# Kernel tuning notes

Measured on AMD Instinct MI355X. Metric: run time of the kernel, lower is better.

Reference implementation:

```python
import jax, jax.numpy as jnp
import numpy as np

TEMPERATURE = 0.07
MARGIN = 0.2
SHUF_ID_OFFSET = 100000


def _normalize(x):
    # matches F.normalize(x + 1e-8, dim=-1) with default eps=1e-12
    v = x + 1e-8
    n = jnp.linalg.norm(v, axis=-1, keepdims=True)
    return v / jnp.maximum(n, 1e-12)


def setup_inputs() -> dict:
    key = jax.random.key(0)
    k1, k2, k3, k4 = jax.random.split(key, 4)
    M, C, D = 1024, 3, 512
    return {
        "motion_embs": jax.random.normal(k1, (M, D), dtype=jnp.float32),
        "text_embs": jax.random.normal(k2, (M, C, D), dtype=jnp.float32),
        "shuffled_text_embs": jax.random.normal(k3, (M, C, D), dtype=jnp.float32),
        "motion_ids": jax.random.randint(k4, (M,), 0, 256, dtype=jnp.int64 if jax.config.jax_enable_x64 else jnp.int32),
    }


def reference(motion_embs, text_embs, shuffled_text_embs, motion_ids):
    M, C, D = text_embs.shape
    m = _normalize(motion_embs)                       # [M, D]
    t = _normalize(text_embs).reshape(M * C, D)       # [M*C, D]
    s = _normalize(shuffled_text_embs).reshape(M * C, D)

    emb = jnp.concatenate([m, t, s], axis=0)          # [N, D], N = M + 2*M*C
    ids = jnp.concatenate([
        motion_ids,
        jnp.repeat(motion_ids, C),
        jnp.repeat(motion_ids + SHUF_ID_OFFSET, C),
    ])

    sim = (emb @ emb.T) / TEMPERATURE                 # [N, N]
    N = emb.shape[0]
    same = ids[None, :] == ids[:, None]
    eye = jnp.eye(N, dtype=bool)
    pos_mask = same & ~eye
    neg_mask = (~same) & ~eye

    exp_sim = jnp.exp(sim)
    # denominator over positives + negatives (all off-diagonal), as in the original
    denom = jnp.sum(jnp.where(pos_mask | neg_mask, exp_sim, 0.0), axis=1)   # [N]
    n_pos = jnp.sum(pos_mask, axis=1)
    n_neg = jnp.sum(neg_mask, axis=1)

    pos_sum = jnp.sum(jnp.where(pos_mask, sim, 0.0), axis=1)
    infonce = jnp.log(denom) - pos_sum / jnp.maximum(n_pos, 1)               # [N]

    margin = jnp.sum(jnp.where(neg_mask, jnp.maximum(sim + MARGIN, 0.0), 0.0), axis=1) / jnp.maximum(n_neg, 1)

    valid = (n_pos > 0) & (n_neg > 0)
    count = jnp.sum(valid)
    total = jnp.sum(jnp.where(valid, infonce + margin, 0.0))
    loss = jnp.where(count > 0, total / jnp.maximum(count, 1), 0.0)
    return loss
```

## Files before the change

kernel.cpp:

```cpp
#include <hip/hip_runtime.h>

#define M_ROWS 1024
#define DIM 512
#define NB 1024
#define N_TOT 7168
#define TEXT_OFF 1024
#define SHUF_OFF 4096
#define INV_T (1.0f/0.07f)
#define MARGIN_V 0.2f
#define TILES2 28
#define NBLK2 406
#define SLOT 1536

typedef __attribute__((ext_vector_type(8))) short bf16x8;
typedef __attribute__((ext_vector_type(4))) float f32x4;

typedef const __attribute__((address_space(1))) unsigned int gas_uint;
typedef __attribute__((address_space(3))) unsigned int las_uint;

__device__ __forceinline__ void gload16(const void* g, void* l) {
  __builtin_amdgcn_global_load_lds((gas_uint*)g, (las_uint*)l, 16, 0, 0);
}

__device__ __forceinline__ ushort f2bf(float f) {
  unsigned u = __float_as_uint(f);
  u += 0x7fffu + ((u >> 16) & 1u);
  return (ushort)(u >> 16);
}

__device__ __forceinline__ float dpp_sum16(float x) {
  float s = x;
  s += __int_as_float(__builtin_amdgcn_update_dpp(0, __float_as_int(s), 0x111, 0xF, 0xF, true));
  s += __int_as_float(__builtin_amdgcn_update_dpp(0, __float_as_int(s), 0x112, 0xF, 0xF, true));
  s += __int_as_float(__builtin_amdgcn_update_dpp(0, __float_as_int(s), 0x114, 0xF, 0xF, true));
  s += __int_as_float(__builtin_amdgcn_update_dpp(0, __float_as_int(s), 0x118, 0xF, 0xF, true));
  return s;
}

__global__ __launch_bounds__(256) void k_normalize(
    const float* __restrict__ motion, const float* __restrict__ text,
    const float* __restrict__ shuf, const int* __restrict__ mids,
    ushort* __restrict__ emb, int* __restrict__ ids) {
  int wave = threadIdx.x >> 6;
  int lane = threadIdx.x & 63;
  int row = blockIdx.x * 4 + wave;
  if (row >= N_TOT) return;
  const float* src;
  int id;
  if (row < TEXT_OFF) { src = motion + (size_t)row * DIM; id = mids[row]; }
  else if (row < SHUF_OFF) { int r = row - TEXT_OFF; src = text + (size_t)r * DIM; id = mids[r / 3]; }
  else { int r = row - SHUF_OFF; src = shuf + (size_t)r * DIM; id = mids[r / 3] + 100000; }

  float4 a = ((const float4*)src)[lane * 2];
  float4 b = ((const float4*)src)[lane * 2 + 1];
  float v0 = a.x + 1e-8f, v1 = a.y + 1e-8f, v2 = a.z + 1e-8f, v3 = a.w + 1e-8f;
  float v4 = b.x + 1e-8f, v5 = b.y + 1e-8f, v6 = b.z + 1e-8f, v7 = b.w + 1e-8f;
  float ss = v0*v0 + v1*v1 + v2*v2 + v3*v3 + v4*v4 + v5*v5 + v6*v6 + v7*v7;
  #pragma unroll
  for (int m = 1; m < 64; m <<= 1) ss += __shfl_xor(ss, m);
  float inv = 1.0f / fmaxf(sqrtf(ss), 1e-12f);

  uint w0 = (uint)f2bf(v0 * inv) | ((uint)f2bf(v1 * inv) << 16);
  uint w1 = (uint)f2bf(v2 * inv) | ((uint)f2bf(v3 * inv) << 16);
  uint w2 = (uint)f2bf(v4 * inv) | ((uint)f2bf(v5 * inv) << 16);
  uint w3 = (uint)f2bf(v6 * inv) | ((uint)f2bf(v7 * inv) << 16);
  uint4 pk; pk.x = w0; pk.y = w1; pk.z = w2; pk.w = w3;
  *((uint4*)(emb + (size_t)row * DIM + lane * 8)) = pk;
  if (lane == 0) ids[row] = id;
}

__global__ __launch_bounds__(512, 2) void k_gemm_loss(
    const ushort* __restrict__ emb, const int* __restrict__ ids,
    float* __restrict__ part) {
  __shared__ ushort Asm[3][8192];
  __shared__ ushort Bsm[3][8192];

  int orig = blockIdx.x;
  int xcd = orig & 7;
  int idx = orig >> 3;
  int bid = (xcd < 6 ? xcd * 51 : 306 + (xcd - 6) * 50) + idx;

  int x = 0;
  while (bid >= TILES2 - x) { bid -= TILES2 - x; x++; }
  int y = x + bid;
  bool diag = (x == y);
  int brow = x * 256, bcol = y * 256;
  int tbid = x * TILES2 - x * (x - 1) / 2 + (y - x);

  int t = threadIdx.x;
  int l = t & 63;
  int w = t >> 6;
  int wr = w >> 2;
  int wc = w & 3;
  int fr = l & 15;
  int fg = l >> 4;

  int srow = w * 16 + (l >> 2);
  int scol = ((l & 3) ^ ((l >> 3) & 3)) * 16;
  const char* gA = (const char*)emb + (size_t)(brow + srow) * NB + scol;
  const char* gB = (const char*)emb + (size_t)(bcol + srow) * NB + scol;
  int ldso = w * 512;

  f32x4 acc[8][4];
  #pragma unroll
  for (int m = 0; m < 8; m++)
    #pragma unroll
    for (int n = 0; n < 4; n++)
      acc[m][n] = (f32x4){0.f, 0.f, 0.f, 0.f};

  int swz = (fg ^ ((fr >> 1) & 3)) * 8;

#define STAGE(T) do { \
    const int _b = (T) % 3; const int _kb = (T) * 64; \
    gload16(gA + _kb,          &Asm[_b][ldso]); \
    gload16(gA + 131072 + _kb, &Asm[_b][4096 + ldso]); \
    gload16(gB + _kb,          &Bsm[_b][ldso]); \
    gload16(gB + 131072 + _kb, &Bsm[_b][4096 + ldso]); \
  } while (0)

  STAGE(0);
  STAGE(1);
  asm volatile("s_waitcnt vmcnt(4)" ::: "memory");
  __builtin_amdgcn_s_barrier();

  #pragma unroll
  for (int tt = 0; tt < 16; tt++) {
    if (tt + 2 < 16) STAGE(tt + 2);
    const int _b = tt % 3;
    const ushort* Ab = &Asm[_b][(wr * 128 + fr) * 32 + swz];
    const ushort* Bb = &Bsm[_b][(wc * 64 + fr) * 32 + swz];
    bf16x8 aF[8], bF[4];
    #pragma unroll
    for (int m = 0; m < 8; m++) aF[m] = *(const bf16x8*)(Ab + m * 512);
    #pragma unroll
    for (int n = 0; n < 4; n++) bF[n] = *(const bf16x8*)(Bb + n * 512);
    __builtin_amdgcn_s_setprio(1);
    #pragma unroll
    for (int m = 0; m < 8; m++)
      #pragma unroll
      for (int n = 0; n < 4; n++)
        acc[m][n] = __builtin_amdgcn_mfma_f32_16x16x32_bf16(aF[m], bF[n], acc[m][n], 0, 0, 0);
    __builtin_amdgcn_s_setprio(0);
    if (tt < 14) {
      asm volatile("s_waitcnt vmcnt(4)" ::: "memory");
      __builtin_amdgcn_s_barrier();
    } else if (tt == 14) {
      asm volatile("s_waitcnt vmcnt(0)" ::: "memory");
      __builtin_amdgcn_s_barrier();
    }
  }
#undef STAGE

  float* rpd = (float*)&Asm[0][0];
  float* rpp = rpd + 1024;
  float* rpm = rpp + 1024;
  float* cps = (float*)&Bsm[0][0];
  int* ridL = (int*)&Bsm[1][0];
  int* cidL = ridL + 256;
  if (t < 256) ridL[t] = ids[brow + t];
  else cidL[t - 256] = ids[bcol + (t - 256)];
  __syncthreads();

  float* ps = part + (size_t)tbid * SLOT;

  int cl = fr;
  int cgrp = fg;
  int cidv[4];
  #pragma unroll
  for (int n = 0; n < 4; n++) cidv[n] = cidL[wc * 64 + n * 16 + cl];
  float cd[4], cp[4], cm[4];
  #pragma unroll
  for (int n = 0; n < 4; n++) { cd[n] = 0.f; cp[n] = 0.f; cm[n] = 0.f; }

  #pragma unroll
  for (int m = 0; m < 8; m++) {
    #pragma unroll
    for (int r = 0; r < 4; r++) {
      int row_l = wr * 128 + m * 16 + cgrp * 4 + r;
      int i = brow + row_l;
      int idi = ridL[row_l];
      float dsum = 0.f, psum = 0.f, msum = 0.f;
      #pragma unroll
      for (int n = 0; n < 4; n++) {
        int col_l = wc * 64 + n * 16 + cl;
        int j = bcol + col_l;
        float sim = acc[m][n][r] * INV_T;
        bool live = (!diag) || (i != j);
        if (live) {
          float e = __expf(sim);
          float hinge = fmaxf(sim + MARGIN_V, 0.f);
          bool same = (idi == cidv[n]);
          float psv = same ? sim : 0.f;
          float msv = same ? 0.f : hinge;
          dsum += e; psum += psv; msum += msv;
          if (!diag) { cd[n] += e; cp[n] += psv; cm[n] += msv; }
        }
      }
      dsum = dpp_sum16(dsum);
      psum = dpp_sum16(psum);
      msum = dpp_sum16(msum);
      if (cl == 15) {
        int o = w * 128 + (row_l & 127);
        rpd[o] = dsum; rpp[o] = psum; rpm[o] = msum;
      }
    }
  }

  if (!diag) {
    #pragma unroll
    for (int n = 0; n < 4; n++) {
      float d = cd[n], p = cp[n], mm = cm[n];
      d += __shfl_xor(d, 16); d += __shfl_xor(d, 32);
      p += __shfl_xor(p, 16); p += __shfl_xor(p, 32);
      mm += __shfl_xor(mm, 16); mm += __shfl_xor(mm, 32);
      if (l < 16) {
        int o = ((w * 4 + n) * 16 + cl) * 3;
        cps[o] = d; cps[o + 1] = p; cps[o + 2] = mm;
      }
    }
  }
  __syncthreads();

  if (t < 256) {
    int b0 = (t >> 7) * 512 + (t & 127);
    float d = rpd[b0] + rpd[b0 + 128] + rpd[b0 + 256] + rpd[b0 + 384];
    float p = rpp[b0] + rpp[b0 + 128] + rpp[b0 + 256] + rpp[b0 + 384];
    float mm = rpm[b0] + rpm[b0 + 128] + rpm[b0 + 256] + rpm[b0 + 384];
    ps[t] = d; ps[256 + t] = p; ps[512 + t] = mm;
  }
  if (!diag && wr == 0 && l < 16) {
    #pragma unroll
    for (int n = 0; n < 4; n++) {
      int o0 = ((w * 4 + n) * 16 + cl) * 3;
      int o1 = (((w + 4) * 4 + n) * 16 + cl) * 3;
      int col_l = wc * 64 + n * 16 + cl;
      ps[768 + col_l] = cps[o0] + cps[o1];
      ps[768 + 256 + col_l] = cps[o0 + 1] + cps[o1 + 1];
      ps[768 + 512 + col_l] = cps[o0 + 2] + cps[o1 + 2];
    }
  }
}

__global__ __launch_bounds__(256) void k_reduce(
    const float* __restrict__ part, const int* __restrict__ mids,
    float* __restrict__ blockout) {
  __shared__ int hist[256];
  __shared__ float reds[256];
  __shared__ int redc[256];
  int t = threadIdx.x;
  hist[t] = 0;
  __syncthreads();
  for (int i = t; i < M_ROWS; i += 256) atomicAdd(&hist[mids[i]], 1);
  __syncthreads();

  int p = blockIdx.x;
  int i = p * 256 + t;
  float d = 0.f, pp = 0.f, mm = 0.f;
  int base = p * TILES2 - p * (p - 1) / 2;
  for (int yy = p; yy < TILES2; yy++) {
    const float* s = part + (size_t)(base + yy - p) * SLOT;
    d += s[t]; pp += s[256 + t]; mm += s[512 + t];
  }
  for (int xx = 0; xx < p; xx++) {
    int b = xx * TILES2 - xx * (xx - 1) / 2 + (p - xx);
    const float* s = part + (size_t)b * SLOT + 768;
    d += s[t]; pp += s[256 + t]; mm += s[512 + t];
  }

  int vmid; bool sh = false;
  if (i < TEXT_OFF) vmid = mids[i];
  else if (i < SHUF_OFF) vmid = mids[(i - TEXT_OFF) / 3];
  else { vmid = mids[(i - SHUF_OFF) / 3]; sh = true; }
  int c = hist[vmid];
  int npos = sh ? (3 * c - 1) : (4 * c - 1);
  int nneg = N_TOT - 1 - npos;
  float val = 0.f; int cnt = 0;
  if (npos > 0 && nneg > 0) {
    val = logf(d) - pp / (float)(npos > 1 ? npos : 1) + mm / (float)(nneg > 1 ? nneg : 1);
    cnt = 1;
  }
  reds[t] = val; redc[t] = cnt;
  __syncthreads();
  for (int s2 = 128; s2 > 0; s2 >>= 1) {
    if (t < s2) { reds[t] += reds[t + s2]; redc[t] += redc[t + s2]; }
    __syncthreads();
  }
  if (t == 0) { blockout[p * 2] = reds[0]; blockout[p * 2 + 1] = (float)redc[0]; }
}

__global__ __launch_bounds__(64) void k_final(
    const float* __restrict__ blockout, float* __restrict__ out) {
  int t = threadIdx.x;
  float s = 0.f, c = 0.f;
  if (t < TILES2) { s = blockout[t * 2]; c = blockout[t * 2 + 1]; }
  #pragma unroll
  for (int m = 32; m > 0; m >>= 1) { s += __shfl_down(s, m); c += __shfl_down(c, m); }
  if (t == 0) out[0] = (c > 0.f) ? s / c : 0.f;
}

extern "C" void kernel_launch(void* const* d_in, const int* in_sizes, int n_in,
                              void* d_out, int out_size, void* d_ws, size_t ws_size,
                              hipStream_t stream) {
  const float* motion = (const float*)d_in[0];
  const float* text   = (const float*)d_in[1];
  const float* shuf   = (const float*)d_in[2];
  const int*   mids   = (const int*)d_in[3];

  char* ws = (char*)d_ws;
  ushort* emb = (ushort*)ws;
  int* ids    = (int*)(ws + (size_t)N_TOT * DIM * 2);
  float* blockout = (float*)(ws + 7368704);
  float* part = (float*)(ws + 7454720);

  k_normalize<<<N_TOT / 4, 256, 0, stream>>>(motion, text, shuf, mids, emb, ids);
  k_gemm_loss<<<NBLK2, 512, 0, stream>>>(emb, ids, part);
  k_reduce<<<TILES2, 256, 0, stream>>>(part, mids, blockout);
  k_final<<<1, 64, 0, stream>>>(blockout, (float*)d_out);
}
```

Before: 74.42 us.

## Shrink GEMM tiles to 128x128 and fuse final reduction via ticket

Halves the symmetric-GEMM tile from 256x256 to 128x128, giving 1596 upper-triangle blocks of 256 threads instead of 406 blocks of 512. This improves load balance and wave coverage across CUs at the cost of less operand reuse per block and more partial-sum traffic. It also folds the final scalar reduction into k_reduce using an atomic ticket, which is reset in k_normalize, so one kernel launch is removed.

```diff
diff --git a/kernel.cpp b/kernel.cpp
--- a/kernel.cpp
+++ b/kernel.cpp
@@ -8,9 +8,9 @@
 #define SHUF_OFF 4096
 #define INV_T (1.0f/0.07f)
 #define MARGIN_V 0.2f
-#define TILES2 28
-#define NBLK2 406
-#define SLOT 1536
+#define TILES 56
+#define NBLK 1596
+#define SLOT 768
 
 typedef __attribute__((ext_vector_type(8))) short bf16x8;
 typedef __attribute__((ext_vector_type(4))) float f32x4;
@@ -40,7 +40,8 @@
 __global__ __launch_bounds__(256) void k_normalize(
     const float* __restrict__ motion, const float* __restrict__ text,
     const float* __restrict__ shuf, const int* __restrict__ mids,
-    ushort* __restrict__ emb, int* __restrict__ ids) {
+    ushort* __restrict__ emb, int* __restrict__ ids, int* __restrict__ ticket) {
+  if (blockIdx.x == 0 && threadIdx.x == 0) *ticket = 0;
   int wave = threadIdx.x >> 6;
   int lane = threadIdx.x & 63;
   int row = blockIdx.x * 4 + wave;
@@ -69,29 +70,29 @@
   if (lane == 0) ids[row] = id;
 }
 
-__global__ __launch_bounds__(512, 2) void k_gemm_loss(
+__global__ __launch_bounds__(256, 3) void k_gemm_loss(
     const ushort* __restrict__ emb, const int* __restrict__ ids,
     float* __restrict__ part) {
-  __shared__ ushort Asm[3][8192];
-  __shared__ ushort Bsm[3][8192];
+  __shared__ ushort Asm[3][4096];
+  __shared__ ushort Bsm[3][4096];
 
   int orig = blockIdx.x;
   int xcd = orig & 7;
   int idx = orig >> 3;
-  int bid = (xcd < 6 ? xcd * 51 : 306 + (xcd - 6) * 50) + idx;
+  int bid = (xcd < 4 ? xcd * 200 : 800 + (xcd - 4) * 199) + idx;
 
   int x = 0;
-  while (bid >= TILES2 - x) { bid -= TILES2 - x; x++; }
+  while (bid >= TILES - x) { bid -= TILES - x; x++; }
   int y = x + bid;
   bool diag = (x == y);
-  int brow = x * 256, bcol = y * 256;
-  int tbid = x * TILES2 - x * (x - 1) / 2 + (y - x);
+  int brow = x * 128, bcol = y * 128;
+  int tbid = x * TILES - x * (x - 1) / 2 + (y - x);
 
   int t = threadIdx.x;
   int l = t & 63;
   int w = t >> 6;
-  int wr = w >> 2;
-  int wc = w & 3;
+  int wr = w >> 1;
+  int wc = w & 1;
   int fr = l & 15;
   int fg = l >> 4;
 
@@ -101,9 +102,9 @@
   const char* gB = (const char*)emb + (size_t)(bcol + srow) * NB + scol;
   int ldso = w * 512;
 
-  f32x4 acc[8][4];
-  #pragma unroll
-  for (int m = 0; m < 8; m++)
+  f32x4 acc[4][4];
+  #pragma unroll
+  for (int m = 0; m < 4; m++)
     #pragma unroll
     for (int n = 0; n < 4; n++)
       acc[m][n] = (f32x4){0.f, 0.f, 0.f, 0.f};
@@ -112,10 +113,10 @@
 
 #define STAGE(T) do { \
     const int _b = (T) % 3; const int _kb = (T) * 64; \
-    gload16(gA + _kb,          &Asm[_b][ldso]); \
-    gload16(gA + 131072 + _kb, &Asm[_b][4096 + ldso]); \
-    gload16(gB + _kb,          &Bsm[_b][ldso]); \
-    gload16(gB + 131072 + _kb, &Bsm[_b][4096 + ldso]); \
+    gload16(gA + _kb,         &Asm[_b][ldso]); \
+    gload16(gA + 65536 + _kb, &Asm[_b][2048 + ldso]); \
+    gload16(gB + _kb,         &Bsm[_b][ldso]); \
+    gload16(gB + 65536 + _kb, &Bsm[_b][2048 + ldso]); \
   } while (0)
 
   STAGE(0);
@@ -127,16 +128,16 @@
   for (int tt = 0; tt < 16; tt++) {
     if (tt + 2 < 16) STAGE(tt + 2);
     const int _b = tt % 3;
-    const ushort* Ab = &Asm[_b][(wr * 128 + fr) * 32 + swz];
+    const ushort* Ab = &Asm[_b][(wr * 64 + fr) * 32 + swz];
     const ushort* Bb = &Bsm[_b][(wc * 64 + fr) * 32 + swz];
-    bf16x8 aF[8], bF[4];
-    #pragma unroll
-    for (int m = 0; m < 8; m++) aF[m] = *(const bf16x8*)(Ab + m * 512);
+    bf16x8 aF[4], bF[4];
+    #pragma unroll
+    for (int m = 0; m < 4; m++) aF[m] = *(const bf16x8*)(Ab + m * 512);
     #pragma unroll
     for (int n = 0; n < 4; n++) bF[n] = *(const bf16x8*)(Bb + n * 512);
     __builtin_amdgcn_s_setprio(1);
     #pragma unroll
-    for (int m = 0; m < 8; m++)
+    for (int m = 0; m < 4; m++)
       #pragma unroll
       for (int n = 0; n < 4; n++)
         acc[m][n] = __builtin_amdgcn_mfma_f32_16x16x32_bf16(aF[m], bF[n], acc[m][n], 0, 0, 0);
@@ -151,14 +152,15 @@
   }
 #undef STAGE
 
-  float* rpd = (float*)&Asm[0][0];
-  float* rpp = rpd + 1024;
-  float* rpm = rpp + 1024;
-  float* cps = (float*)&Bsm[0][0];
-  int* ridL = (int*)&Bsm[1][0];
-  int* cidL = ridL + 256;
-  if (t < 256) ridL[t] = ids[brow + t];
-  else cidL[t - 256] = ids[bcol + (t - 256)];
+  __syncthreads();
+  float* rpd = (float*)&Asm[1][0];
+  float* rpp = rpd + 256;
+  float* rpm = rpp + 256;
+  float* cps = (float*)&Bsm[1][0];
+  int* ridL = (int*)&Asm[2][0];
+  int* cidL = ridL + 128;
+  if (t < 128) ridL[t] = ids[brow + t];
+  else cidL[t - 128] = ids[bcol + (t - 128)];
   __syncthreads();
 
   float* ps = part + (size_t)tbid * SLOT;
@@ -173,10 +175,10 @@
   for (int n = 0; n < 4; n++) { cd[n] = 0.f; cp[n] = 0.f; cm[n] = 0.f; }
 
   #pragma unroll
-  for (int m = 0; m < 8; m++) {
+  for (int m = 0; m < 4; m++) {
     #pragma unroll
     for (int r = 0; r < 4; r++) {
-      int row_l = wr * 128 + m * 16 + cgrp * 4 + r;
+      int row_l = wr * 64 + m * 16 + cgrp * 4 + r;
       int i = brow + row_l;
       int idi = ridL[row_l];
       float dsum = 0.f, psum = 0.f, msum = 0.f;
@@ -200,7 +202,7 @@
       psum = dpp_sum16(psum);
       msum = dpp_sum16(msum);
       if (cl == 15) {
-        int o = w * 128 + (row_l & 127);
+        int o = w * 64 + (row_l & 63);
         rpd[o] = dsum; rpp[o] = psum; rpm[o] = msum;
       }
     }
@@ -221,50 +223,52 @@
   }
   __syncthreads();
 
-  if (t < 256) {
-    int b0 = (t >> 7) * 512 + (t & 127);
-    float d = rpd[b0] + rpd[b0 + 128] + rpd[b0 + 256] + rpd[b0 + 384];
-    float p = rpp[b0] + rpp[b0 + 128] + rpp[b0 + 256] + rpp[b0 + 384];
-    float mm = rpm[b0] + rpm[b0 + 128] + rpm[b0 + 256] + rpm[b0 + 384];
-    ps[t] = d; ps[256 + t] = p; ps[512 + t] = mm;
+  if (t < 128) {
+    int b0 = (t >> 6) * 128 + (t & 63);
+    float d = rpd[b0] + rpd[b0 + 64];
+    float p = rpp[b0] + rpp[b0 + 64];
+    float mm = rpm[b0] + rpm[b0 + 64];
+    ps[t] = d; ps[128 + t] = p; ps[256 + t] = mm;
   }
   if (!diag && wr == 0 && l < 16) {
     #pragma unroll
     for (int n = 0; n < 4; n++) {
       int o0 = ((w * 4 + n) * 16 + cl) * 3;
-      int o1 = (((w + 4) * 4 + n) * 16 + cl) * 3;
-      int col_l = wc * 64 + n * 16 + cl;
-      ps[768 + col_l] = cps[o0] + cps[o1];
-      ps[768 + 256 + col_l] = cps[o0 + 1] + cps[o1 + 1];
-      ps[768 + 512 + col_l] = cps[o0 + 2] + cps[o1 + 2];
-    }
-  }
-}
-
-__global__ __launch_bounds__(256) void k_reduce(
+      int o1 = (((w + 2) * 4 + n) * 16 + cl) * 3;
+      int col_l = w * 64 + n * 16 + cl;
+      ps[384 + col_l] = cps[o0] + cps[o1];
+      ps[384 + 128 + col_l] = cps[o0 + 1] + cps[o1 + 1];
+      ps[384 + 256 + col_l] = cps[o0 + 2] + cps[o1 + 2];
+    }
+  }
+}
+
+__global__ __launch_bounds__(128) void k_reduce(
     const float* __restrict__ part, const int* __restrict__ mids,
-    float* __restrict__ blockout) {
+    float* __restrict__ blockout, int* __restrict__ ticket,
+    float* __restrict__ out) {
   __shared__ int hist[256];
-  __shared__ float reds[256];
-  __shared__ int redc[256];
+  __shared__ float reds[128];
+  __shared__ int redc[128];
+  __shared__ int lastf;
   int t = threadIdx.x;
-  hist[t] = 0;
-  __syncthreads();
-  for (int i = t; i < M_ROWS; i += 256) atomicAdd(&hist[mids[i]], 1);
+  hist[t] = 0; hist[t + 128] = 0;
+  __syncthreads();
+  for (int i = t; i < M_ROWS; i += 128) atomicAdd(&hist[mids[i]], 1);
   __syncthreads();
 
   int p = blockIdx.x;
-  int i = p * 256 + t;
+  int i = p * 128 + t;
   float d = 0.f, pp = 0.f, mm = 0.f;
-  int base = p * TILES2 - p * (p - 1) / 2;
-  for (int yy = p; yy < TILES2; yy++) {
+  int base = p * TILES - p * (p - 1) / 2;
+  for (int yy = p; yy < TILES; yy++) {
     const float* s = part + (size_t)(base + yy - p) * SLOT;
-    d += s[t]; pp += s[256 + t]; mm += s[512 + t];
+    d += s[t]; pp += s[128 + t]; mm += s[256 + t];
   }
   for (int xx = 0; xx < p; xx++) {
-    int b = xx * TILES2 - xx * (xx - 1) / 2 + (p - xx);
-    const float* s = part + (size_t)b * SLOT + 768;
-    d += s[t]; pp += s[256 + t]; mm += s[512 + t];
+    int b = xx * TILES - xx * (xx - 1) / 2 + (p - xx);
+    const float* s = part + (size_t)b * SLOT + 384;
+    d += s[t]; pp += s[128 + t]; mm += s[256 + t];
   }
 
   int vmid; bool sh = false;
@@ -281,21 +285,30 @@
   }
   reds[t] = val; redc[t] = cnt;
   __syncthreads();
-  for (int s2 = 128; s2 > 0; s2 >>= 1) {
+  for (int s2 = 64; s2 > 0; s2 >>= 1) {
     if (t < s2) { reds[t] += reds[t + s2]; redc[t] += redc[t + s2]; }
     __syncthreads();
   }
-  if (t == 0) { blockout[p * 2] = reds[0]; blockout[p * 2 + 1] = (float)redc[0]; }
-}
-
-__global__ __launch_bounds__(64) void k_final(
-    const float* __restrict__ blockout, float* __restrict__ out) {
-  int t = threadIdx.x;
-  float s = 0.f, c = 0.f;
-  if (t < TILES2) { s = blockout[t * 2]; c = blockout[t * 2 + 1]; }
-  #pragma unroll
-  for (int m = 32; m > 0; m >>= 1) { s += __shfl_down(s, m); c += __shfl_down(c, m); }
-  if (t == 0) out[0] = (c > 0.f) ? s / c : 0.f;
+  if (t == 0) {
+    blockout[p * 2] = reds[0];
+    blockout[p * 2 + 1] = (float)redc[0];
+    __threadfence();
+    int old = atomicAdd(ticket, 1);
+    lastf = (old == TILES - 1);
+  }
+  __syncthreads();
+  if (lastf) {
+    __threadfence();
+    float s = (t < TILES) ? blockout[t * 2] : 0.f;
+    float cc = (t < TILES) ? blockout[t * 2 + 1] : 0.f;
+    reds[t] = s; redc[t] = (int)cc;
+    __syncthreads();
+    for (int s2 = 64; s2 > 0; s2 >>= 1) {
+      if (t < s2) { reds[t] += reds[t + s2]; redc[t] += redc[t + s2]; }
+      __syncthreads();
+    }
+    if (t == 0) out[0] = (redc[0] > 0) ? reds[0] / (float)redc[0] : 0.f;
+  }
 }
 
 extern "C" void kernel_launch(void* const* d_in, const int* in_sizes, int n_in,
@@ -308,12 +321,12 @@
 
   char* ws = (char*)d_ws;
   ushort* emb = (ushort*)ws;
-  int* ids    = (int*)(ws + (size_t)N_TOT * DIM * 2);
+  int* ids    = (int*)(ws + 7340032);
   float* blockout = (float*)(ws + 7368704);
-  float* part = (float*)(ws + 7454720);
-
-  k_normalize<<<N_TOT / 4, 256, 0, stream>>>(motion, text, shuf, mids, emb, ids);
-  k_gemm_loss<<<NBLK2, 512, 0, stream>>>(emb, ids, part);
-  k_reduce<<<TILES2, 256, 0, stream>>>(part, mids, blockout);
-  k_final<<<1, 64, 0, stream>>>(blockout, (float*)d_out);
-}
+  int* ticket = (int*)(ws + 7369216);
+  float* part = (float*)(ws + 7372800);
+
+  k_normalize<<<N_TOT / 4, 256, 0, stream>>>(motion, text, shuf, mids, emb, ids, ticket);
+  k_gemm_loss<<<NBLK, 256, 0, stream>>>(emb, ids, part);
+  k_reduce<<<TILES, 128, 0, stream>>>(part, mids, blockout, ticket, (float*)d_out);
+}
```

Result: slower. 81.14 us (+9.0%).

## Restructure GEMM mainloop into K=128 double-buffered stages with interleaved quarter-MFMA schedule

Applied to the files above, without the earlier changes.

Replaces the 3-stage K=64 LDS ring with a 2-stage double buffer of K=128 tiles, split into halves, and issues global-to-LDS loads for the next tile between quarter-sized MFMA groups separated by barriers. The aim is finer interleaving of memory loads with matrix work and fewer barrier/waitcnt rounds per K step. LDS use rises to 128KB, so launch bounds drop to one block per CU, trading occupancy for deeper in-block pipelining. The swizzle is widened to 8 chunks to match the new 128-element row layout.

```diff
diff --git a/kernel.cpp b/kernel.cpp
--- a/kernel.cpp
+++ b/kernel.cpp
@@ -69,11 +69,11 @@
   if (lane == 0) ids[row] = id;
 }
 
-__global__ __launch_bounds__(512, 2) void k_gemm_loss(
+__global__ __launch_bounds__(512, 1) void k_gemm_loss(
     const ushort* __restrict__ emb, const int* __restrict__ ids,
     float* __restrict__ part) {
-  __shared__ ushort Asm[3][8192];
-  __shared__ ushort Bsm[3][8192];
+  __shared__ ushort Asm[2][2][8192];
+  __shared__ ushort Bsm[2][2][8192];
 
   int orig = blockIdx.x;
   int xcd = orig & 7;
@@ -95,11 +95,10 @@
   int fr = l & 15;
   int fg = l >> 4;
 
-  int srow = w * 16 + (l >> 2);
-  int scol = ((l & 3) ^ ((l >> 3) & 3)) * 16;
-  const char* gA = (const char*)emb + (size_t)(brow + srow) * NB + scol;
-  const char* gB = (const char*)emb + (size_t)(bcol + srow) * NB + scol;
-  int ldso = w * 512;
+  int srow = w * 8 + (l >> 3);
+  int sgb = ((l & 7) ^ ((l >> 3) & 7)) * 16;
+  const char* gAr = (const char*)emb + (size_t)(brow + srow) * NB + sgb;
+  const char* gBr = (const char*)emb + (size_t)(bcol + srow) * NB + sgb;
 
   f32x4 acc[8][4];
   #pragma unroll
@@ -108,54 +107,96 @@
     for (int n = 0; n < 4; n++)
       acc[m][n] = (f32x4){0.f, 0.f, 0.f, 0.f};
 
-  int swz = (fg ^ ((fr >> 1) & 3)) * 8;
-
-#define STAGE(T) do { \
-    const int _b = (T) % 3; const int _kb = (T) * 64; \
-    gload16(gA + _kb,          &Asm[_b][ldso]); \
-    gload16(gA + 131072 + _kb, &Asm[_b][4096 + ldso]); \
-    gload16(gB + _kb,          &Bsm[_b][ldso]); \
-    gload16(gB + 131072 + _kb, &Bsm[_b][4096 + ldso]); \
+  int sw0 = ((fg) ^ (fr & 7)) * 8;
+  int sw1 = ((4 + fg) ^ (fr & 7)) * 8;
+
+#define STAGE_A(H, KT) do { \
+    gload16(gAr + (size_t)(H) * 131072 + (KT) * 128,         &Asm[(KT) & 1][H][w * 512]); \
+    gload16(gAr + (size_t)(H) * 131072 + 65536 + (KT) * 128, &Asm[(KT) & 1][H][4096 + w * 512]); \
   } while (0)
-
-  STAGE(0);
-  STAGE(1);
-  asm volatile("s_waitcnt vmcnt(4)" ::: "memory");
-  __builtin_amdgcn_s_barrier();
-
-  #pragma unroll
-  for (int tt = 0; tt < 16; tt++) {
-    if (tt + 2 < 16) STAGE(tt + 2);
-    const int _b = tt % 3;
-    const ushort* Ab = &Asm[_b][(wr * 128 + fr) * 32 + swz];
-    const ushort* Bb = &Bsm[_b][(wc * 64 + fr) * 32 + swz];
-    bf16x8 aF[8], bF[4];
-    #pragma unroll
-    for (int m = 0; m < 8; m++) aF[m] = *(const bf16x8*)(Ab + m * 512);
-    #pragma unroll
-    for (int n = 0; n < 4; n++) bF[n] = *(const bf16x8*)(Bb + n * 512);
-    __builtin_amdgcn_s_setprio(1);
-    #pragma unroll
-    for (int m = 0; m < 8; m++)
-      #pragma unroll
-      for (int n = 0; n < 4; n++)
-        acc[m][n] = __builtin_amdgcn_mfma_f32_16x16x32_bf16(aF[m], bF[n], acc[m][n], 0, 0, 0);
-    __builtin_amdgcn_s_setprio(0);
-    if (tt < 14) {
-      asm volatile("s_waitcnt vmcnt(4)" ::: "memory");
-      __builtin_amdgcn_s_barrier();
-    } else if (tt == 14) {
-      asm volatile("s_waitcnt vmcnt(0)" ::: "memory");
-      __builtin_amdgcn_s_barrier();
-    }
-  }
-#undef STAGE
-
-  float* rpd = (float*)&Asm[0][0];
+#define STAGE_B(H, KT) do { \
+    gload16(gBr + (size_t)(H) * 131072 + (KT) * 128,         &Bsm[(KT) & 1][H][w * 512]); \
+    gload16(gBr + (size_t)(H) * 131072 + 65536 + (KT) * 128, &Bsm[(KT) & 1][H][4096 + w * 512]); \
+  } while (0)
+
+  bf16x8 aF[4][2], bF0[2][2], bF1[2][2];
+
+#define LOAD_A(KT, MH) do { \
+    const ushort* AH = &Asm[(KT) & 1][wr][0]; \
+    _Pragma("unroll") \
+    for (int mi = 0; mi < 4; mi++) { \
+      int ro = (((MH) * 4 + mi) * 16 + fr) * 64; \
+      aF[mi][0] = *(const bf16x8*)(AH + ro + sw0); \
+      aF[mi][1] = *(const bf16x8*)(AH + ro + sw1); \
+    } } while (0)
+#define LOAD_B(KT, NH, DST) do { \
+    const ushort* BH = &Bsm[(KT) & 1][wc >> 1][0]; \
+    _Pragma("unroll") \
+    for (int ni = 0; ni < 2; ni++) { \
+      int ro = ((wc & 1) * 64 + ((NH) * 2 + ni) * 16 + fr) * 64; \
+      DST[ni][0] = *(const bf16x8*)(BH + ro + sw0); \
+      DST[ni][1] = *(const bf16x8*)(BH + ro + sw1); \
+    } } while (0)
+#define MFMA_Q(MH, NH, BSRC) do { \
+    __builtin_amdgcn_s_setprio(1); \
+    _Pragma("unroll") \
+    for (int ks = 0; ks < 2; ks++) \
+      _Pragma("unroll") \
+      for (int mi = 0; mi < 4; mi++) \
+        _Pragma("unroll") \
+        for (int ni = 0; ni < 2; ni++) \
+          acc[(MH) * 4 + mi][(NH) * 2 + ni] = __builtin_amdgcn_mfma_f32_16x16x32_bf16( \
+              aF[mi][ks], BSRC[ni][ks], acc[(MH) * 4 + mi][(NH) * 2 + ni], 0, 0, 0); \
+    __builtin_amdgcn_s_setprio(0); \
+  } while (0)
+#define BAR() __builtin_amdgcn_s_barrier()
+#define DRAIN() do { asm volatile("s_waitcnt vmcnt(0)" ::: "memory"); __builtin_amdgcn_s_barrier(); } while (0)
+
+  STAGE_A(0, 0); STAGE_A(1, 0); STAGE_B(0, 0); STAGE_B(1, 0);
+  DRAIN();
+
+  #pragma unroll
+  for (int it = 0; it < 4; it++) {
+    const int ka = 2 * it, kb = 2 * it + 1;
+    LOAD_A(ka, 0); LOAD_B(ka, 0, bF0);
+    STAGE_A(0, kb);
+    BAR(); MFMA_Q(0, 0, bF0); BAR();
+    LOAD_B(ka, 1, bF1);
+    STAGE_A(1, kb);
+    BAR(); MFMA_Q(0, 1, bF1); BAR();
+    LOAD_A(ka, 1);
+    STAGE_B(0, kb);
+    BAR(); MFMA_Q(1, 0, bF0); BAR();
+    STAGE_B(1, kb);
+    BAR(); MFMA_Q(1, 1, bF1);
+    DRAIN();
+    LOAD_A(kb, 0); LOAD_B(kb, 0, bF0);
+    if (it < 3) STAGE_A(0, ka + 2);
+    BAR(); MFMA_Q(0, 0, bF0); BAR();
+    LOAD_B(kb, 1, bF1);
+    if (it < 3) STAGE_A(1, ka + 2);
+    BAR(); MFMA_Q(0, 1, bF1); BAR();
+    LOAD_A(kb, 1);
+    if (it < 3) STAGE_B(0, ka + 2);
+    BAR(); MFMA_Q(1, 0, bF0); BAR();
+    if (it < 3) STAGE_B(1, ka + 2);
+    BAR(); MFMA_Q(1, 1, bF1);
+    DRAIN();
+  }
+#undef STAGE_A
+#undef STAGE_B
+#undef LOAD_A
+#undef LOAD_B
+#undef MFMA_Q
+#undef BAR
+#undef DRAIN
+
+  __syncthreads();
+  float* rpd = (float*)&Asm[0][0][0];
   float* rpp = rpd + 1024;
   float* rpm = rpp + 1024;
-  float* cps = (float*)&Bsm[0][0];
-  int* ridL = (int*)&Bsm[1][0];
+  float* cps = (float*)&Bsm[0][0][0];
+  int* ridL = (int*)&Bsm[1][0][0];
   int* cidL = ridL + 256;
   if (t < 256) ridL[t] = ids[brow + t];
   else cidL[t - 256] = ids[bcol + (t - 256)];
@@ -308,7 +349,7 @@
 
   char* ws = (char*)d_ws;
   ushort* emb = (ushort*)ws;
-  int* ids    = (int*)(ws + (size_t)N_TOT * DIM * 2);
+  int* ids    = (int*)(ws + 7340032);
   float* blockout = (float*)(ws + 7368704);
   float* part = (float*)(ws + 7454720);
 
```

After: 75.29 us. About the same (+1.2%).

## Quantize embeddings to FP8 and use FP8 MFMA for similarity GEMM

Applied to the files above, without the earlier changes.

Normalized embeddings are stored as packed FP8 instead of bf16, halving the embedding buffer and global-to-LDS traffic. The GEMM switches to fp8 MFMA 16x16x32 with a new LDS layout and swizzle, and runs half as many k-steps. The reduce kernel is split into 56 blocks of 128 threads to spread the work. FP8 precision on similarities scaled by 1/0.07 and then exponentiated risks accuracy loss against the reference.

```diff
diff --git a/kernel.cpp b/kernel.cpp
--- a/kernel.cpp
+++ b/kernel.cpp
@@ -2,7 +2,7 @@
 
 #define M_ROWS 1024
 #define DIM 512
-#define NB 1024
+#define NB 512
 #define N_TOT 7168
 #define TEXT_OFF 1024
 #define SHUF_OFF 4096
@@ -12,7 +12,6 @@
 #define NBLK2 406
 #define SLOT 1536
 
-typedef __attribute__((ext_vector_type(8))) short bf16x8;
 typedef __attribute__((ext_vector_type(4))) float f32x4;
 
 typedef const __attribute__((address_space(1))) unsigned int gas_uint;
@@ -20,12 +19,6 @@
 
 __device__ __forceinline__ void gload16(const void* g, void* l) {
   __builtin_amdgcn_global_load_lds((gas_uint*)g, (las_uint*)l, 16, 0, 0);
-}
-
-__device__ __forceinline__ ushort f2bf(float f) {
-  unsigned u = __float_as_uint(f);
-  u += 0x7fffu + ((u >> 16) & 1u);
-  return (ushort)(u >> 16);
 }
 
 __device__ __forceinline__ float dpp_sum16(float x) {
@@ -40,7 +33,7 @@
 __global__ __launch_bounds__(256) void k_normalize(
     const float* __restrict__ motion, const float* __restrict__ text,
     const float* __restrict__ shuf, const int* __restrict__ mids,
-    ushort* __restrict__ emb, int* __restrict__ ids) {
+    unsigned char* __restrict__ emb, int* __restrict__ ids) {
   int wave = threadIdx.x >> 6;
   int lane = threadIdx.x & 63;
   int row = blockIdx.x * 4 + wave;
@@ -60,20 +53,20 @@
   for (int m = 1; m < 64; m <<= 1) ss += __shfl_xor(ss, m);
   float inv = 1.0f / fmaxf(sqrtf(ss), 1e-12f);
 
-  uint w0 = (uint)f2bf(v0 * inv) | ((uint)f2bf(v1 * inv) << 16);
-  uint w1 = (uint)f2bf(v2 * inv) | ((uint)f2bf(v3 * inv) << 16);
-  uint w2 = (uint)f2bf(v4 * inv) | ((uint)f2bf(v5 * inv) << 16);
-  uint w3 = (uint)f2bf(v6 * inv) | ((uint)f2bf(v7 * inv) << 16);
-  uint4 pk; pk.x = w0; pk.y = w1; pk.z = w2; pk.w = w3;
-  *((uint4*)(emb + (size_t)row * DIM + lane * 8)) = pk;
+  int w0 = __builtin_amdgcn_cvt_pk_fp8_f32(v0 * inv, v1 * inv, 0, false);
+  w0     = __builtin_amdgcn_cvt_pk_fp8_f32(v2 * inv, v3 * inv, w0, true);
+  int w1 = __builtin_amdgcn_cvt_pk_fp8_f32(v4 * inv, v5 * inv, 0, false);
+  w1     = __builtin_amdgcn_cvt_pk_fp8_f32(v6 * inv, v7 * inv, w1, true);
+  uint2 pk; pk.x = (unsigned)w0; pk.y = (unsigned)w1;
+  *((uint2*)(emb + (size_t)row * NB + lane * 8)) = pk;
   if (lane == 0) ids[row] = id;
 }
 
 __global__ __launch_bounds__(512, 2) void k_gemm_loss(
-    const ushort* __restrict__ emb, const int* __restrict__ ids,
+    const unsigned char* __restrict__ emb, const int* __restrict__ ids,
     float* __restrict__ part) {
-  __shared__ ushort Asm[3][8192];
-  __shared__ ushort Bsm[3][8192];
+  __shared__ unsigned char Asm[3][16384];
+  __shared__ unsigned char Bsm[3][16384];
 
   int orig = blockIdx.x;
   int xcd = orig & 7;
@@ -99,7 +92,7 @@
   int scol = ((l & 3) ^ ((l >> 3) & 3)) * 16;
   const char* gA = (const char*)emb + (size_t)(brow + srow) * NB + scol;
   const char* gB = (const char*)emb + (size_t)(bcol + srow) * NB + scol;
-  int ldso = w * 512;
+  int ldso = w * 1024;
 
   f32x4 acc[8][4];
   #pragma unroll
@@ -108,14 +101,14 @@
     for (int n = 0; n < 4; n++)
       acc[m][n] = (f32x4){0.f, 0.f, 0.f, 0.f};
 
-  int swz = (fg ^ ((fr >> 1) & 3)) * 8;
+  int rsw = (fr >> 1) & 3;
 
 #define STAGE(T) do { \
     const int _b = (T) % 3; const int _kb = (T) * 64; \
-    gload16(gA + _kb,          &Asm[_b][ldso]); \
-    gload16(gA + 131072 + _kb, &Asm[_b][4096 + ldso]); \
-    gload16(gB + _kb,          &Bsm[_b][ldso]); \
-    gload16(gB + 131072 + _kb, &Bsm[_b][4096 + ldso]); \
+    gload16(gA + _kb,         &Asm[_b][ldso]); \
+    gload16(gA + 65536 + _kb, &Asm[_b][8192 + ldso]); \
+    gload16(gB + _kb,         &Bsm[_b][ldso]); \
+    gload16(gB + 65536 + _kb, &Bsm[_b][8192 + ldso]); \
   } while (0)
 
   STAGE(0);
@@ -124,27 +117,34 @@
   __builtin_amdgcn_s_barrier();
 
   #pragma unroll
-  for (int tt = 0; tt < 16; tt++) {
-    if (tt + 2 < 16) STAGE(tt + 2);
+  for (int tt = 0; tt < 8; tt++) {
+    if (tt + 2 < 8) STAGE(tt + 2);
     const int _b = tt % 3;
-    const ushort* Ab = &Asm[_b][(wr * 128 + fr) * 32 + swz];
-    const ushort* Bb = &Bsm[_b][(wc * 64 + fr) * 32 + swz];
-    bf16x8 aF[8], bF[4];
-    #pragma unroll
-    for (int m = 0; m < 8; m++) aF[m] = *(const bf16x8*)(Ab + m * 512);
-    #pragma unroll
-    for (int n = 0; n < 4; n++) bF[n] = *(const bf16x8*)(Bb + n * 512);
-    __builtin_amdgcn_s_setprio(1);
-    #pragma unroll
-    for (int m = 0; m < 8; m++)
+    long aF[8][2], bF[4][2];
+    #pragma unroll
+    for (int kh = 0; kh < 2; kh++) {
+      int g0 = kh * 4 + fg;
+      int goff = (((g0 >> 1) ^ rsw) * 16) + (g0 & 1) * 8;
+      #pragma unroll
+      for (int m = 0; m < 8; m++)
+        aF[m][kh] = *(const long*)(&Asm[_b][(wr * 128 + m * 16 + fr) * 64 + goff]);
       #pragma unroll
       for (int n = 0; n < 4; n++)
-        acc[m][n] = __builtin_amdgcn_mfma_f32_16x16x32_bf16(aF[m], bF[n], acc[m][n], 0, 0, 0);
+        bF[n][kh] = *(const long*)(&Bsm[_b][(wc * 64 + n * 16 + fr) * 64 + goff]);
+    }
+    __builtin_amdgcn_s_setprio(1);
+    #pragma unroll
+    for (int kh = 0; kh < 2; kh++)
+      #pragma unroll
+      for (int m = 0; m < 8; m++)
+        #pragma unroll
+        for (int n = 0; n < 4; n++)
+          acc[m][n] = __builtin_amdgcn_mfma_f32_16x16x32_fp8_fp8(aF[m][kh], bF[n][kh], acc[m][n], 0, 0, 0);
     __builtin_amdgcn_s_setprio(0);
-    if (tt < 14) {
+    if (tt < 6) {
       asm volatile("s_waitcnt vmcnt(4)" ::: "memory");
       __builtin_amdgcn_s_barrier();
-    } else if (tt == 14) {
+    } else if (tt == 6) {
       asm volatile("s_waitcnt vmcnt(0)" ::: "memory");
       __builtin_amdgcn_s_barrier();
     }
@@ -155,7 +155,7 @@
   float* rpp = rpd + 1024;
   float* rpm = rpp + 1024;
   float* cps = (float*)&Bsm[0][0];
-  int* ridL = (int*)&Bsm[1][0];
+  int* ridL = (int*)&Asm[2][0];
   int* cidL = ridL + 256;
   if (t < 256) ridL[t] = ids[brow + t];
   else cidL[t - 256] = ids[bcol + (t - 256)];
@@ -241,30 +241,31 @@
   }
 }
 
-__global__ __launch_bounds__(256) void k_reduce(
+__global__ __launch_bounds__(128) void k_reduce(
     const float* __restrict__ part, const int* __restrict__ mids,
     float* __restrict__ blockout) {
   __shared__ int hist[256];
-  __shared__ float reds[256];
-  __shared__ int redc[256];
+  __shared__ float reds[128];
+  __shared__ int redc[128];
   int t = threadIdx.x;
-  hist[t] = 0;
-  __syncthreads();
-  for (int i = t; i < M_ROWS; i += 256) atomicAdd(&hist[mids[i]], 1);
-  __syncthreads();
-
-  int p = blockIdx.x;
-  int i = p * 256 + t;
+  hist[t] = 0; hist[t + 128] = 0;
+  __syncthreads();
+  for (int i = t; i < M_ROWS; i += 128) atomicAdd(&hist[mids[i]], 1);
+  __syncthreads();
+
+  int i = blockIdx.x * 128 + t;
+  int p = blockIdx.x >> 1;
+  int v = i & 255;
   float d = 0.f, pp = 0.f, mm = 0.f;
   int base = p * TILES2 - p * (p - 1) / 2;
   for (int yy = p; yy < TILES2; yy++) {
     const float* s = part + (size_t)(base + yy - p) * SLOT;
-    d += s[t]; pp += s[256 + t]; mm += s[512 + t];
+    d += s[v]; pp += s[256 + v]; mm += s[512 + v];
   }
   for (int xx = 0; xx < p; xx++) {
     int b = xx * TILES2 - xx * (xx - 1) / 2 + (p - xx);
     const float* s = part + (size_t)b * SLOT + 768;
-    d += s[t]; pp += s[256 + t]; mm += s[512 + t];
+    d += s[v]; pp += s[256 + v]; mm += s[512 + v];
   }
 
   int vmid; bool sh = false;
@@ -281,18 +282,18 @@
   }
   reds[t] = val; redc[t] = cnt;
   __syncthreads();
-  for (int s2 = 128; s2 > 0; s2 >>= 1) {
+  for (int s2 = 64; s2 > 0; s2 >>= 1) {
     if (t < s2) { reds[t] += reds[t + s2]; redc[t] += redc[t + s2]; }
     __syncthreads();
   }
-  if (t == 0) { blockout[p * 2] = reds[0]; blockout[p * 2 + 1] = (float)redc[0]; }
+  if (t == 0) { blockout[blockIdx.x * 2] = reds[0]; blockout[blockIdx.x * 2 + 1] = (float)redc[0]; }
 }
 
 __global__ __launch_bounds__(64) void k_final(
     const float* __restrict__ blockout, float* __restrict__ out) {
   int t = threadIdx.x;
   float s = 0.f, c = 0.f;
-  if (t < TILES2) { s = blockout[t * 2]; c = blockout[t * 2 + 1]; }
+  if (t < 56) { s = blockout[t * 2]; c = blockout[t * 2 + 1]; }
   #pragma unroll
   for (int m = 32; m > 0; m >>= 1) { s += __shfl_down(s, m); c += __shfl_down(c, m); }
   if (t == 0) out[0] = (c > 0.f) ? s / c : 0.f;
@@ -307,13 +308,13 @@
   const int*   mids   = (const int*)d_in[3];
 
   char* ws = (char*)d_ws;
-  ushort* emb = (ushort*)ws;
-  int* ids    = (int*)(ws + (size_t)N_TOT * DIM * 2);
-  float* blockout = (float*)(ws + 7368704);
-  float* part = (float*)(ws + 7454720);
+  unsigned char* emb = (unsigned char*)ws;
+  int* ids    = (int*)(ws + 3670016);
+  float* blockout = (float*)(ws + 3698688);
+  float* part = (float*)(ws + 3702784);
 
   k_normalize<<<N_TOT / 4, 256, 0, stream>>>(motion, text, shuf, mids, emb, ids);
   k_gemm_loss<<<NBLK2, 512, 0, stream>>>(emb, ids, part);
-  k_reduce<<<TILES2, 256, 0, stream>>>(part, mids, blockout);
+  k_reduce<<<56, 128, 0, stream>>>(part, mids, blockout);
   k_final<<<1, 64, 0, stream>>>(blockout, (float*)d_out);
 }
```

Result: faster. 72.58 us (-2.5%).
